# Kernel optimization log

Hardware: AMD Instinct MI355X
Metric: run time of the kernel (lower is better)

## Reference

```python
import jax, jax.numpy as jnp
import numpy as np

H = 256  # hidden_size
D = 256  # in_vocab_size
T = 512  # sequence length


def setup_inputs() -> dict:
    key = jax.random.key(0)
    k1, k2, k3, k4, k5 = jax.random.split(key, 5)
    # faithful param init from the torch module
    u1 = jax.random.uniform(k1, (H,), minval=1e-4, maxval=1.0)
    u2 = jax.random.uniform(k2, (H,), minval=1e-4, maxval=1.0)
    lamda = jnp.log(-0.5 * jnp.log(u1))
    theta = jnp.log(6.28 * u2)
    B_c1 = jax.random.normal(k3, (H, D), dtype=jnp.float32) / np.float32(np.sqrt(D))
    B_c2 = jax.random.normal(k4, (H, D), dtype=jnp.float32) / np.float32(np.sqrt(D))
    x_sequence = jax.random.normal(k5, (T, D), dtype=jnp.float32)
    return {"x_sequence": x_sequence, "lamda": lamda, "theta": theta,
            "B_c1": B_c1, "B_c2": B_c2}


def reference(x_sequence, lamda, theta, B_c1, B_c2):
    Hh = lamda.shape[0]
    Dd = B_c1.shape[1]
    # per-step constant coefficients (depend only on params)
    y = jnp.exp(-jnp.exp(lamda))
    z = jnp.exp(theta)
    gamma = jnp.sqrt(1.0 - y * y)
    cz, sz = jnp.cos(z), jnp.sin(z)
    c, s = y * cz, y * sz                       # rotation coefficients [H]
    y_g = -jnp.exp(lamda) * y                   # dy/dlamda
    gamma_g = -y / gamma * y_g                  # dgamma/dlamda
    z_g = jnp.exp(theta)                        # dz/dtheta
    # precompute input projections for all steps: [T, H]
    Bx1 = x_sequence @ B_c1.T
    Bx2 = x_sequence @ B_c2.T

    def step(carry, xs):
        h1, h2, sr1, sr2, st1, st2, sB11, sB12, sB21, sB22 = carry
        x_t, bx1, bx2 = xs
        # hidden state (complex diagonal rotation, split into 2 real channels)
        h1n = c * h1 - s * h2 + gamma * bx1
        h2n = c * h2 + s * h1 + gamma * bx2
        # RTRL sensitivities w.r.t. lamda
        sr1n = y_g * cz * h1 + c * sr1 - y_g * sz * h2 - s * sr2 + gamma_g * bx1
        sr2n = y_g * cz * h2 + c * sr2 + y_g * sz * h1 + s * sr1 + gamma_g * bx2
        # RTRL sensitivities w.r.t. theta
        st1n = -s * z_g * h1 + c * st1 - c * z_g * h2 - s * st2
        st2n = -s * z_g * h2 + c * st2 + c * z_g * h1 + s * st1
        # RTRL sensitivities w.r.t. B matrices, [H, D]
        gx = gamma[:, None] * x_t[None, :]
        sB11n = c[:, None] * sB11 - s[:, None] * sB12 + gx
        sB12n = c[:, None] * sB12 + s[:, None] * sB11
        sB21n = c[:, None] * sB21 - s[:, None] * sB22
        sB22n = c[:, None] * sB22 + s[:, None] * sB21 + gx
        out = jnp.concatenate([h1n, h2n])       # [2H]
        return (h1n, h2n, sr1n, sr2n, st1n, st2n, sB11n, sB12n, sB21n, sB22n), out

    zv = jnp.zeros((Hh,), jnp.float32)
    zm = jnp.zeros((Hh, Dd), jnp.float32)
    init = (zv, zv, zv, zv, zv, zv, zm, zm, zm, zm)
    _, outs = jax.lax.scan(step, init, (x_sequence, Bx1, Bx2))
    return outs  # [T, 2H]
```

## Files before the change

kernel.cpp:

```cpp
#include <hip/hip_runtime.h>

#define TT 512
#define DD 256
#define HH 256

#define CC 32
#define LL (TT / CC)
#define USPLIT 8
#define UPB (HH / USPLIT)
#define KSPLIT 8
#define KW (DD / KSPLIT)

__device__ inline void coeffs(const float* __restrict__ lamda,
                              const float* __restrict__ theta, int j,
                              float& c, float& s, float& g) {
  const float y = __expf(-__expf(lamda[j]));
  const float z = __expf(theta[j]);
  c = y * __cosf(z);
  s = y * __sinf(z);
  g = sqrtf(fmaxf(1.0f - y * y, 0.0f));
}

__global__ __launch_bounds__(256) void rtu_chunk(
    const float* __restrict__ x, const float* __restrict__ lamda,
    const float* __restrict__ theta, const float* __restrict__ B1,
    const float* __restrict__ B2, float* __restrict__ out,
    float* __restrict__ E) {
  __shared__ float xs[LL * DD];
  const int cidx = blockIdx.x >> 3;
  const int q = blockIdx.x & (USPLIT - 1);
  const int t0 = cidx * LL;
  const int tid = threadIdx.x;
  const int ul = tid >> 3;
  const int kq = tid & (KSPLIT - 1);
  const int u = q * UPB + ul;

  {
    const float4* xsrc = (const float4*)(x + t0 * DD);
    float4* xdst = (float4*)xs;
#pragma unroll
    for (int p = 0; p < (LL * DD / 4) / 256; ++p)
      xdst[p * 256 + tid] = xsrc[p * 256 + tid];
  }
  __syncthreads();

  const float4* b1 = (const float4*)(B1 + u * DD + kq * KW);
  const float4* b2 = (const float4*)(B2 + u * DD + kq * KW);
  const float4* xs4 = (const float4*)xs;

  float a1[LL], a2[LL];
#pragma unroll
  for (int tt = 0; tt < LL; ++tt) { a1[tt] = 0.f; a2[tt] = 0.f; }

#pragma unroll
  for (int k4 = 0; k4 < KW / 4; ++k4) {
    const int kk = (k4 + kq) & (KW / 4 - 1);
    const float4 v1 = b1[kk];
    const float4 v2 = b2[kk];
#pragma unroll
    for (int tt = 0; tt < LL; ++tt) {
      const float4 xv = xs4[tt * (DD / 4) + kq * (KW / 4) + kk];
      a1[tt] = fmaf(v1.x, xv.x, a1[tt]);
      a1[tt] = fmaf(v1.y, xv.y, a1[tt]);
      a1[tt] = fmaf(v1.z, xv.z, a1[tt]);
      a1[tt] = fmaf(v1.w, xv.w, a1[tt]);
      a2[tt] = fmaf(v2.x, xv.x, a2[tt]);
      a2[tt] = fmaf(v2.y, xv.y, a2[tt]);
      a2[tt] = fmaf(v2.z, xv.z, a2[tt]);
      a2[tt] = fmaf(v2.w, xv.w, a2[tt]);
    }
  }

#pragma unroll
  for (int tt = 0; tt < LL; ++tt) {
    float r1 = a1[tt], r2 = a2[tt];
    r1 += __shfl_xor(r1, 1);
    r1 += __shfl_xor(r1, 2);
    r1 += __shfl_xor(r1, 4);
    r2 += __shfl_xor(r2, 1);
    r2 += __shfl_xor(r2, 2);
    r2 += __shfl_xor(r2, 4);
    a1[tt] = r1;
    a2[tt] = r2;
  }

  float c, s, g;
  coeffs(lamda, theta, u, c, s, g);

  float h1 = 0.f, h2 = 0.f;
#pragma unroll
  for (int tt = 0; tt < LL; ++tt) {
    const float bb1 = a1[tt] * g;
    const float bb2 = a2[tt] * g;
    const float n1 = fmaf(c, h1, fmaf(-s, h2, bb1));
    const float n2 = fmaf(c, h2, fmaf(s, h1, bb2));
    h1 = n1;
    h2 = n2;
    if (kq == (tt >> 1)) {
      out[(t0 + tt) * (2 * HH) + u] = h1;
      out[(t0 + tt) * (2 * HH) + HH + u] = h2;
    }
  }
  if (kq == 0) E[cidx * (2 * HH) + u] = h1;
  if (kq == 1) E[cidx * (2 * HH) + HH + u] = h2;
}

__global__ __launch_bounds__(256) void rtu_fixup(
    const float* __restrict__ lamda, const float* __restrict__ theta,
    const float* __restrict__ E, float* __restrict__ out) {
  const int cidx = blockIdx.x;
  if (cidx == 0) return;
  const int j = threadIdx.x;
  float c, s, g;
  coeffs(lamda, theta, j, c, s, g);

  float cl = c, sl = s;
#pragma unroll
  for (int qq = 0; qq < 4; ++qq) {
    const float nc = cl * cl - sl * sl;
    const float ns = 2.f * cl * sl;
    cl = nc;
    sl = ns;
  }

  float S1 = 0.f, S2 = 0.f;
  const float* Ep = E + j;
#pragma unroll 8
  for (int ci = 0; ci < cidx; ++ci) {
    const float E1 = Ep[ci * (2 * HH)];
    const float E2 = Ep[ci * (2 * HH) + HH];
    const float n1 = fmaf(cl, S1, fmaf(-sl, S2, E1));
    const float n2 = fmaf(cl, S2, fmaf(sl, S1, E2));
    S1 = n1;
    S2 = n2;
  }

  const int t0 = cidx * LL;
  float p1 = c, p2 = s;
#pragma unroll
  for (int i = 0; i < LL; ++i) {
    const int t = t0 + i;
    const float o1 = out[t * (2 * HH) + j] + p1 * S1 - p2 * S2;
    const float o2 = out[t * (2 * HH) + HH + j] + p2 * S1 + p1 * S2;
    out[t * (2 * HH) + j] = o1;
    out[t * (2 * HH) + HH + j] = o2;
    const float np1 = p1 * c - p2 * s;
    const float np2 = p1 * s + p2 * c;
    p1 = np1;
    p2 = np2;
  }
}

extern "C" void kernel_launch(void* const* d_in, const int* in_sizes, int n_in,
                              void* d_out, int out_size, void* d_ws, size_t ws_size,
                              hipStream_t stream) {
  const float* x     = (const float*)d_in[0];
  const float* lamda = (const float*)d_in[1];
  const float* theta = (const float*)d_in[2];
  const float* B1    = (const float*)d_in[3];
  const float* B2    = (const float*)d_in[4];
  float* out = (float*)d_out;

  float* E = (float*)d_ws;

  rtu_chunk<<<dim3(CC * USPLIT), 256, 0, stream>>>(x, lamda, theta, B1, B2,
                                                   out, E);
  rtu_fixup<<<dim3(CC), 256, 0, stream>>>(lamda, theta, E, out);
}
```

Baseline: 78.13 us.

## Fuse chunk scan and carry fixup into one cooperative kernel with grid sync

```diff
diff --git a/kernel.cpp b/kernel.cpp
--- a/kernel.cpp
+++ b/kernel.cpp
@@ -1,4 +1,7 @@
 #include <hip/hip_runtime.h>
+#include <hip/hip_cooperative_groups.h>
+
+namespace cg = cooperative_groups;
 
 #define TT 512
 #define DD 256
@@ -21,7 +24,7 @@
   g = sqrtf(fmaxf(1.0f - y * y, 0.0f));
 }
 
-__global__ __launch_bounds__(256) void rtu_chunk(
+__global__ __launch_bounds__(256) void rtu_fused(
     const float* __restrict__ x, const float* __restrict__ lamda,
     const float* __restrict__ theta, const float* __restrict__ B1,
     const float* __restrict__ B2, float* __restrict__ out,
@@ -35,6 +38,16 @@
   const int kq = tid & (KSPLIT - 1);
   const int u = q * UPB + ul;
 
+  const float4* b1 = (const float4*)(B1 + u * DD + kq * KW);
+  const float4* b2 = (const float4*)(B2 + u * DD + kq * KW);
+  float4 rb1[KW / 4], rb2[KW / 4];
+#pragma unroll
+  for (int k4 = 0; k4 < KW / 4; ++k4) {
+    const int kk = (k4 + kq) & (KW / 4 - 1);
+    rb1[k4] = b1[kk];
+    rb2[k4] = b2[kk];
+  }
+
   {
     const float4* xsrc = (const float4*)(x + t0 * DD);
     float4* xdst = (float4*)xs;
@@ -44,8 +57,6 @@
   }
   __syncthreads();
 
-  const float4* b1 = (const float4*)(B1 + u * DD + kq * KW);
-  const float4* b2 = (const float4*)(B2 + u * DD + kq * KW);
   const float4* xs4 = (const float4*)xs;
 
   float a1[LL], a2[LL];
@@ -55,8 +66,8 @@
 #pragma unroll
   for (int k4 = 0; k4 < KW / 4; ++k4) {
     const int kk = (k4 + kq) & (KW / 4 - 1);
-    const float4 v1 = b1[kk];
-    const float4 v2 = b2[kk];
+    const float4 v1 = rb1[k4];
+    const float4 v2 = rb2[k4];
 #pragma unroll
     for (int tt = 0; tt < LL; ++tt) {
       const float4 xv = xs4[tt * (DD / 4) + kq * (KW / 4) + kk];
@@ -88,6 +99,7 @@
   coeffs(lamda, theta, u, c, s, g);
 
   float h1 = 0.f, h2 = 0.f;
+  float l1a = 0.f, l2a = 0.f, l1b = 0.f, l2b = 0.f;
 #pragma unroll
   for (int tt = 0; tt < LL; ++tt) {
     const float bb1 = a1[tt] * g;
@@ -97,22 +109,16 @@
     h1 = n1;
     h2 = n2;
     if (kq == (tt >> 1)) {
-      out[(t0 + tt) * (2 * HH) + u] = h1;
-      out[(t0 + tt) * (2 * HH) + HH + u] = h2;
+      if (tt & 1) { l1b = h1; l2b = h2; }
+      else        { l1a = h1; l2a = h2; }
     }
   }
   if (kq == 0) E[cidx * (2 * HH) + u] = h1;
   if (kq == 1) E[cidx * (2 * HH) + HH + u] = h2;
-}
 
-__global__ __launch_bounds__(256) void rtu_fixup(
-    const float* __restrict__ lamda, const float* __restrict__ theta,
-    const float* __restrict__ E, float* __restrict__ out) {
-  const int cidx = blockIdx.x;
-  if (cidx == 0) return;
-  const int j = threadIdx.x;
-  float c, s, g;
-  coeffs(lamda, theta, j, c, s, g);
+  __threadfence();
+  cg::this_grid().sync();
+  __threadfence();
 
   float cl = c, sl = s;
 #pragma unroll
@@ -124,7 +130,7 @@
   }
 
   float S1 = 0.f, S2 = 0.f;
-  const float* Ep = E + j;
+  const float* Ep = E + u;
 #pragma unroll 8
   for (int ci = 0; ci < cidx; ++ci) {
     const float E1 = Ep[ci * (2 * HH)];
@@ -135,20 +141,25 @@
     S2 = n2;
   }
 
-  const int t0 = cidx * LL;
   float p1 = c, p2 = s;
+  float pa1 = 0.f, pa2 = 0.f, pb1 = 0.f, pb2 = 0.f;
 #pragma unroll
   for (int i = 0; i < LL; ++i) {
-    const int t = t0 + i;
-    const float o1 = out[t * (2 * HH) + j] + p1 * S1 - p2 * S2;
-    const float o2 = out[t * (2 * HH) + HH + j] + p2 * S1 + p1 * S2;
-    out[t * (2 * HH) + j] = o1;
-    out[t * (2 * HH) + HH + j] = o2;
+    if (kq == (i >> 1)) {
+      if (i & 1) { pb1 = p1; pb2 = p2; }
+      else       { pa1 = p1; pa2 = p2; }
+    }
     const float np1 = p1 * c - p2 * s;
     const float np2 = p1 * s + p2 * c;
     p1 = np1;
     p2 = np2;
   }
+
+  const int ta = t0 + 2 * kq;
+  out[ta * (2 * HH) + u]            = l1a + pa1 * S1 - pa2 * S2;
+  out[ta * (2 * HH) + HH + u]       = l2a + pa2 * S1 + pa1 * S2;
+  out[(ta + 1) * (2 * HH) + u]      = l1b + pb1 * S1 - pb2 * S2;
+  out[(ta + 1) * (2 * HH) + HH + u] = l2b + pb2 * S1 + pb1 * S2;
 }
 
 extern "C" void kernel_launch(void* const* d_in, const int* in_sizes, int n_in,
@@ -163,7 +174,8 @@
 
   float* E = (float*)d_ws;
 
-  rtu_chunk<<<dim3(CC * USPLIT), 256, 0, stream>>>(x, lamda, theta, B1, B2,
-                                                   out, E);
-  rtu_fixup<<<dim3(CC), 256, 0, stream>>>(lamda, theta, E, out);
+  void* args[] = {(void*)&x, (void*)&lamda, (void*)&theta,
+                  (void*)&B1, (void*)&B2, (void*)&out, (void*)&E};
+  hipLaunchCooperativeKernel((const void*)rtu_fused, dim3(CC * USPLIT),
+                             dim3(256), args, 0, stream);
 }
```

Result: slower. 133.7 us (+71.1%).
